# Performance work log

Measured on AMD Instinct MI355X. Metric: run time of the kernel, lower is better.

The kernel has to match this reference:

```python
import jax, jax.numpy as jnp
import numpy as np

# Config derived from layers=[1024,1024,1024,1024,1024]
B = 16384      # batch
H1 = 1024      # layers[1], width of first odd layer (Ux target slice)
SE = 2048      # sum of even-layer dims (0 + 1024 + 1024)
SO = 2048      # sum of odd-layer dims (1024 + 1024)
LAYER = 1024
N_STEPS = 10


def rho(x):
    return jax.nn.sigmoid(4.0 * (x - 0.5))


def rhod(x):
    r = rho(x)
    return 4.0 * r * (1.0 - r)


def _block_mask():
    # Staircase blocks per layer_slices(): (0:1024,0:1024), (0:1024,1024:2048), (1024:2048,1024:2048)
    m = np.zeros((SE, SO), dtype=np.float32)
    m[0:LAYER, 0:LAYER] = 1.0
    m[0:LAYER, LAYER:2 * LAYER] = 1.0
    m[LAYER:2 * LAYER, LAYER:2 * LAYER] = 1.0
    return jnp.asarray(m)


def setup_inputs() -> dict:
    key = jax.random.key(0)
    k1, k2, k3, k4, k5 = jax.random.split(key, 5)
    Ux = jax.random.normal(k1, (B, H1), dtype=jnp.float32)
    s = jax.random.normal(k2, (B, SE + SO), dtype=jnp.float32)
    # Xavier uniform per 1024x1024 block: bound = sqrt(6 / (1024 + 1024))
    bound = (6.0 / (2 * LAYER)) ** 0.5
    W = jax.random.uniform(k3, (SE, SO), minval=-bound, maxval=bound, dtype=jnp.float32) * _block_mask()
    b_even = 0.01 * jax.random.normal(k4, (1, SE), dtype=jnp.float32)
    b_odd = 0.01 * jax.random.normal(k5, (1, SO), dtype=jnp.float32)
    return {"Ux": Ux, "s": s, "W": W, "b_even": b_even, "b_odd": b_odd}


def reference(Ux, s, W, b_even, b_odd):
    s_even, s_odd = s[:, :SE], s[:, SE:]
    # C_odd = rho(s_even) @ W + b_odd ; first odd layer also receives Ux
    C_odd = rho(s_even) @ W + b_odd
    C_odd = C_odd.at[:, :H1].add(Ux)
    for _ in range(N_STEPS):
        s_odd = 0.5 * s_odd + 0.5 * rhod(s_odd) * C_odd
    C_even = rho(s_odd) @ W.T + b_even
    for _ in range(N_STEPS):
        s_even = 0.5 * s_even + 0.5 * rhod(s_even) * C_even
    return jnp.concatenate([s_even, s_odd], axis=-1)
```

## Files before the change

kernel.cpp:

```cpp
#include <hip/hip_runtime.h>
#include <hip/hip_bf16.h>

#define BATCH 16384
#define SEW   2048
#define H1W   1024
#define NSTEP 10

typedef unsigned short u16;
typedef __attribute__((ext_vector_type(8))) __bf16 bf16x8;
typedef __attribute__((ext_vector_type(4))) float   f32x4;

__device__ __forceinline__ void split2(float x, u16& h, u16& l) {
    unsigned u = __float_as_uint(x);
    h = (u16)(u >> 16);
    float hf = __uint_as_float(u & 0xFFFF0000u);
    float r  = x - hf;
    l = (u16)(__float_as_uint(r) >> 16);
}

__device__ __forceinline__ float rho_f(float x) {
    return 1.0f / (1.0f + __expf(2.0f - 4.0f * x));
}

__device__ __forceinline__ void gl2lds16(const u16* g, u16* l) {
    __builtin_amdgcn_global_load_lds(
        (const __attribute__((address_space(1))) void*)g,
        (__attribute__((address_space(3))) void*)l, 16, 0, 0);
}

__global__ void prep_w(const float* __restrict__ W,
                       u16* __restrict__ Whi, u16* __restrict__ Wlo,
                       u16* __restrict__ WThi, u16* __restrict__ WTlo) {
    __shared__ float tile[32][33];
    const int tx = threadIdx.x, ty = threadIdx.y;
    const int x = blockIdx.x * 32 + tx;
#pragma unroll
    for (int k = 0; k < 4; ++k) {
        int y = blockIdx.y * 32 + ty + k * 8;
        float v = W[y * SEW + x];
        tile[ty + k * 8][tx] = v;
        u16 h, l; split2(v, h, l);
        Whi[y * SEW + x] = h; Wlo[y * SEW + x] = l;
    }
    __syncthreads();
#pragma unroll
    for (int k = 0; k < 4; ++k) {
        int r = blockIdx.x * 32 + ty + k * 8;
        int c = blockIdx.y * 32 + tx;
        float v = tile[tx][ty + k * 8];
        u16 h, l; split2(v, h, l);
        WThi[r * SEW + c] = h; WTlo[r * SEW + c] = l;
    }
}

__global__ void prep_rho(const float* __restrict__ s,
                         u16* __restrict__ Rhi, u16* __restrict__ Rlo) {
    int i = blockIdx.x * blockDim.x + threadIdx.x;
    int e = i << 2;
    int row = e >> 11;
    int col = e & 2047;
    const float4 v = *(const float4*)(s + ((size_t)row << 12) + col);
    float xs[4] = {v.x, v.y, v.z, v.w};
    u16 h[4], l[4];
#pragma unroll
    for (int k = 0; k < 4; ++k) {
        float r = rho_f(xs[k]);
        split2(r, h[k], l[k]);
    }
    *(ushort4*)(Rhi + e) = make_ushort4(h[0], h[1], h[2], h[3]);
    *(ushort4*)(Rlo + e) = make_ushort4(l[0], l[1], l[2], l[3]);
}

template <int PHASE>
__global__ __launch_bounds__(256, 2)
void gemm_fused(const u16* __restrict__ Ahi, const u16* __restrict__ Alo,
                const u16* __restrict__ Bhi, const u16* __restrict__ Blo,
                const float* __restrict__ bias,
                const float* __restrict__ Ux,
                const float* __restrict__ s_in,
                float* __restrict__ out,
                u16* __restrict__ R2hi, u16* __restrict__ R2lo) {
    __shared__ u16 lsAh[128 * 32], lsAl[128 * 32], lsBh[128 * 32], lsBl[128 * 32];

    const int tid = threadIdx.x;
    const int m0 = blockIdx.x * 128;
    const int n0 = blockIdx.y * 128;

    int k0, k1;
    if (PHASE == 1) { k0 = 0;                      k1 = (n0 < 1024) ? 1024 : 2048; }
    else            { k0 = (n0 < 1024) ? 0 : 1024; k1 = 2048; }

    const int p0 = tid, p1 = tid + 256;
    const int r0 = p0 >> 2, r1 = p1 >> 2;
    const int g0 = (p0 & 3) ^ ((r0 >> 1) & 3);
    const int g1 = (p1 & 3) ^ ((r1 >> 1) & 3);
    const int aoff0 = (m0 + r0) * SEW + g0 * 8;
    const int aoff1 = (m0 + r1) * SEW + g1 * 8;
    const int boff0 = (n0 + r0) * SEW + g0 * 8;
    const int boff1 = (n0 + r1) * SEW + g1 * 8;

    const int lane = tid & 63;
    const int w = tid >> 6;
    const int wr = w >> 1, wc = w & 1;
    const int q = lane >> 4, lr = lane & 15;
    int offA[4], offB[4];
#pragma unroll
    for (int i = 0; i < 4; ++i) {
        int row = wr * 64 + i * 16 + lr;
        offA[i] = row * 64 + ((q ^ ((row >> 1) & 3)) << 4);
        row = wc * 64 + i * 16 + lr;
        offB[i] = row * 64 + ((q ^ ((row >> 1) & 3)) << 4);
    }

    f32x4 acc[4][4];
    const f32x4 zero = {0.f, 0.f, 0.f, 0.f};
#pragma unroll
    for (int i = 0; i < 4; ++i)
#pragma unroll
        for (int j = 0; j < 4; ++j) acc[i][j] = zero;

    const int nk = (k1 - k0) >> 5;
    for (int kt = 0; kt < nk; ++kt) {
        const int kb = k0 + (kt << 5);
        __syncthreads();
        gl2lds16(Ahi + aoff0 + kb, lsAh + p0 * 8);
        gl2lds16(Ahi + aoff1 + kb, lsAh + p1 * 8);
        gl2lds16(Alo + aoff0 + kb, lsAl + p0 * 8);
        gl2lds16(Alo + aoff1 + kb, lsAl + p1 * 8);
        gl2lds16(Bhi + boff0 + kb, lsBh + p0 * 8);
        gl2lds16(Bhi + boff1 + kb, lsBh + p1 * 8);
        gl2lds16(Blo + boff0 + kb, lsBl + p0 * 8);
        gl2lds16(Blo + boff1 + kb, lsBl + p1 * 8);
        __syncthreads();

        bf16x8 ah[4], al[4], bh[4], bl[4];
#pragma unroll
        for (int i = 0; i < 4; ++i) {
            ah[i] = *(const bf16x8*)((const char*)lsAh + offA[i]);
            al[i] = *(const bf16x8*)((const char*)lsAl + offA[i]);
            bh[i] = *(const bf16x8*)((const char*)lsBh + offB[i]);
            bl[i] = *(const bf16x8*)((const char*)lsBl + offB[i]);
        }
#pragma unroll
        for (int i = 0; i < 4; ++i)
#pragma unroll
            for (int j = 0; j < 4; ++j) {
                acc[i][j] = __builtin_amdgcn_mfma_f32_16x16x32_bf16(ah[i], bh[j], acc[i][j], 0, 0, 0);
                acc[i][j] = __builtin_amdgcn_mfma_f32_16x16x32_bf16(ah[i], bl[j], acc[i][j], 0, 0, 0);
                acc[i][j] = __builtin_amdgcn_mfma_f32_16x16x32_bf16(al[i], bh[j], acc[i][j], 0, 0, 0);
            }
    }

#pragma unroll
    for (int i = 0; i < 4; ++i) {
#pragma unroll
        for (int j = 0; j < 4; ++j) {
            const int col = n0 + wc * 64 + j * 16 + lr;
            const float bv = bias[col];
            float c[4], sv[4];
#pragma unroll
            for (int jj = 0; jj < 4; ++jj) {
                const int row = m0 + wr * 64 + i * 16 + q * 4 + jj;
                c[jj] = acc[i][j][jj] + bv;
                if (PHASE == 1) {
                    if (n0 < 1024) c[jj] += Ux[(size_t)row * H1W + col];
                }
                sv[jj] = s_in[(size_t)row * 4096 + col];
            }
#pragma unroll 1
            for (int t = 0; t < NSTEP; ++t) {
#pragma unroll
                for (int jj = 0; jj < 4; ++jj) {
                    float r  = rho_f(sv[jj]);
                    float rd = 4.0f * r * (1.0f - r);
                    sv[jj] = 0.5f * sv[jj] + 0.5f * rd * c[jj];
                }
            }
#pragma unroll
            for (int jj = 0; jj < 4; ++jj) {
                const int row = m0 + wr * 64 + i * 16 + q * 4 + jj;
                out[(size_t)row * 4096 + col] = sv[jj];
                if (PHASE == 1) {
                    float r = rho_f(sv[jj]);
                    u16 h, l; split2(r, h, l);
                    R2hi[row * SEW + col] = h;
                    R2lo[row * SEW + col] = l;
                }
            }
        }
    }
}

extern "C" void kernel_launch(void* const* d_in, const int* in_sizes, int n_in,
                              void* d_out, int out_size, void* d_ws, size_t ws_size,
                              hipStream_t stream) {
    (void)in_sizes; (void)n_in; (void)out_size; (void)ws_size;
    const float* Ux     = (const float*)d_in[0];
    const float* s      = (const float*)d_in[1];
    const float* W      = (const float*)d_in[2];
    const float* b_even = (const float*)d_in[3];
    const float* b_odd  = (const float*)d_in[4];
    float* out = (float*)d_out;

    char* ws = (char*)d_ws;
    const size_t MB = 1024ull * 1024ull;
    u16* R1hi = (u16*)(ws);
    u16* R1lo = (u16*)(ws + 64 * MB);
    u16* R2hi = (u16*)(ws + 128 * MB);
    u16* R2lo = (u16*)(ws + 192 * MB);
    u16* Whi  = (u16*)(ws + 256 * MB);
    u16* Wlo  = (u16*)(ws + 264 * MB);
    u16* WThi = (u16*)(ws + 272 * MB);
    u16* WTlo = (u16*)(ws + 280 * MB);

    prep_w<<<dim3(64, 64), dim3(32, 8), 0, stream>>>(W, Whi, Wlo, WThi, WTlo);
    prep_rho<<<(BATCH * SEW / 4) / 256, 256, 0, stream>>>(s, R1hi, R1lo);

    gemm_fused<1><<<dim3(128, 16), 256, 0, stream>>>(
        R1hi, R1lo, WThi, WTlo, b_odd, Ux,
        s + SEW, out + SEW, R2hi, R2lo);

    gemm_fused<2><<<dim3(128, 16), 256, 0, stream>>>(
        R2hi, R2lo, Whi, Wlo, b_even, nullptr,
        s, out, nullptr, nullptr);
}
```

Before: 1.378 ms.

## Use 256x256 tiles with double-buffered LDS, K=64 stages and XCD-aware block remap

The fused GEMM moves from 128x128 tiles with 256 threads to 256x256 tiles with 512 threads. Each wave now holds an 8x4 accumulator block, and the K dimension is staged 64 wide through double-buffered LDS. The three hi/lo split products are turned into a stream of virtual K tiles (hi*hi, hi*lo, lo*hi), so each stage loads a single A/B pair and the next stage's loads overlap the current MFMAs via vmcnt waits. A 1D grid is remapped so neighbouring tiles land on the same XCD, and s_setprio is raised around the MFMA bursts. The aim is more data reuse per byte loaded and less barrier stall, at the cost of more registers, 128KB of LDS, fewer blocks and possibly lower occupancy.

Measured after the change: 1.606 ms. 1.17x slower.

```diff
diff --git a/kernel.cpp b/kernel.cpp
--- a/kernel.cpp
+++ b/kernel.cpp
@@ -72,7 +72,7 @@
 }
 
 template <int PHASE>
-__global__ __launch_bounds__(256, 2)
+__global__ __launch_bounds__(512, 2)
 void gemm_fused(const u16* __restrict__ Ahi, const u16* __restrict__ Alo,
                 const u16* __restrict__ Bhi, const u16* __restrict__ Blo,
                 const float* __restrict__ bias,
@@ -80,88 +80,143 @@
                 const float* __restrict__ s_in,
                 float* __restrict__ out,
                 u16* __restrict__ R2hi, u16* __restrict__ R2lo) {
-    __shared__ u16 lsAh[128 * 32], lsAl[128 * 32], lsBh[128 * 32], lsBl[128 * 32];
+    __shared__ u16 ldsA[2][256 * 64];
+    __shared__ u16 ldsB[2][256 * 64];
 
     const int tid = threadIdx.x;
-    const int m0 = blockIdx.x * 128;
-    const int n0 = blockIdx.y * 128;
-
-    int k0, k1;
-    if (PHASE == 1) { k0 = 0;                      k1 = (n0 < 1024) ? 1024 : 2048; }
-    else            { k0 = (n0 < 1024) ? 0 : 1024; k1 = 2048; }
-
-    const int p0 = tid, p1 = tid + 256;
-    const int r0 = p0 >> 2, r1 = p1 >> 2;
-    const int g0 = (p0 & 3) ^ ((r0 >> 1) & 3);
-    const int g1 = (p1 & 3) ^ ((r1 >> 1) & 3);
-    const int aoff0 = (m0 + r0) * SEW + g0 * 8;
-    const int aoff1 = (m0 + r1) * SEW + g1 * 8;
-    const int boff0 = (n0 + r0) * SEW + g0 * 8;
-    const int boff1 = (n0 + r1) * SEW + g1 * 8;
+
+    const int wg = blockIdx.x;
+    const int L  = (wg & 7) * 64 + (wg >> 3);
+    const int m0 = (L >> 3) * 256;
+    const int n0 = (L & 7) * 256;
+
+    int kt0, nkt;
+    if (PHASE == 1) { kt0 = 0;                    nkt = (n0 < 1024) ? 16 : 32; }
+    else            { kt0 = (n0 < 1024) ? 0 : 16; nkt = (n0 < 1024) ? 32 : 16; }
+    const int nvt = 3 * nkt;
+
+    const int srow  = tid >> 3;
+    const int sswz  = (tid >> 4) & 7;
+    const int scol  = ((tid & 7) ^ sswz) * 8;
+    const int aoff0 = (m0 + srow) * SEW + scol;
+    const int boff0 = (n0 + srow) * SEW + scol;
 
     const int lane = tid & 63;
-    const int w = tid >> 6;
-    const int wr = w >> 1, wc = w & 1;
-    const int q = lane >> 4, lr = lane & 15;
-    int offA[4], offB[4];
-#pragma unroll
-    for (int i = 0; i < 4; ++i) {
-        int row = wr * 64 + i * 16 + lr;
-        offA[i] = row * 64 + ((q ^ ((row >> 1) & 3)) << 4);
-        row = wc * 64 + i * 16 + lr;
-        offB[i] = row * 64 + ((q ^ ((row >> 1) & 3)) << 4);
-    }
-
-    f32x4 acc[4][4];
+    const int w  = tid >> 6;
+    const int wr = w >> 2, wc = w & 3;
+    const int lr = lane & 15, q = lane >> 4;
+    const int swz = (lr >> 1) & 7;
+    const int oh0 = ((q)     ^ swz) * 16;
+    const int oh1 = ((4 + q) ^ swz) * 16;
+    const int baseA = (wr * 128 + lr) * 128;
+    const int baseB = (wc * 64  + lr) * 128;
+
+    f32x4 acc[8][4];
     const f32x4 zero = {0.f, 0.f, 0.f, 0.f};
 #pragma unroll
-    for (int i = 0; i < 4; ++i)
+    for (int i = 0; i < 8; ++i)
 #pragma unroll
         for (int j = 0; j < 4; ++j) acc[i][j] = zero;
 
-    const int nk = (k1 - k0) >> 5;
-    for (int kt = 0; kt < nk; ++kt) {
-        const int kb = k0 + (kt << 5);
-        __syncthreads();
-        gl2lds16(Ahi + aoff0 + kb, lsAh + p0 * 8);
-        gl2lds16(Ahi + aoff1 + kb, lsAh + p1 * 8);
-        gl2lds16(Alo + aoff0 + kb, lsAl + p0 * 8);
-        gl2lds16(Alo + aoff1 + kb, lsAl + p1 * 8);
-        gl2lds16(Bhi + boff0 + kb, lsBh + p0 * 8);
-        gl2lds16(Bhi + boff1 + kb, lsBh + p1 * 8);
-        gl2lds16(Blo + boff0 + kb, lsBl + p0 * 8);
-        gl2lds16(Blo + boff1 + kb, lsBl + p1 * 8);
-        __syncthreads();
-
-        bf16x8 ah[4], al[4], bh[4], bl[4];
+#define STAGE(As, Bs, kk, buf) do {                                          \
+        u16* dA_ = &ldsA[buf][tid * 8];                                      \
+        u16* dB_ = &ldsB[buf][tid * 8];                                      \
+        const u16* sa_ = (As) + aoff0 + (kk);                                \
+        const u16* sb_ = (Bs) + boff0 + (kk);                                \
+        _Pragma("unroll")                                                    \
+        for (int i_ = 0; i_ < 4; ++i_) {                                     \
+            gl2lds16(sa_ + i_ * (64 * SEW), dA_ + i_ * 4096);                \
+            gl2lds16(sb_ + i_ * (64 * SEW), dB_ + i_ * 4096);                \
+        }                                                                    \
+    } while (0)
+
+    int skk = kt0 * 64;
+    int st  = 1;
+    STAGE(Ahi, Bhi, skk, 0);
+
+    for (int vt = 0; vt < nvt; ++vt) {
+        const int cur = vt & 1;
+        if (vt + 1 < nvt) {
+            const u16* As = (st < 2)  ? Ahi : Alo;
+            const u16* Bs = (st == 1) ? Blo : Bhi;
+            STAGE(As, Bs, skk, cur ^ 1);
+            if (++st == 3) { st = 0; skk += 64; }
+            asm volatile("s_waitcnt vmcnt(8)" ::: "memory");
+        } else {
+            asm volatile("s_waitcnt vmcnt(0)" ::: "memory");
+        }
+        __builtin_amdgcn_s_barrier();
+
+        const char* la = (const char*)ldsA[cur];
+        const char* lb = (const char*)ldsB[cur];
+        bf16x8 av[4][2], bv[4][2];
 #pragma unroll
         for (int i = 0; i < 4; ++i) {
-            ah[i] = *(const bf16x8*)((const char*)lsAh + offA[i]);
-            al[i] = *(const bf16x8*)((const char*)lsAl + offA[i]);
-            bh[i] = *(const bf16x8*)((const char*)lsBh + offB[i]);
-            bl[i] = *(const bf16x8*)((const char*)lsBl + offB[i]);
-        }
-#pragma unroll
-        for (int i = 0; i < 4; ++i)
-#pragma unroll
-            for (int j = 0; j < 4; ++j) {
-                acc[i][j] = __builtin_amdgcn_mfma_f32_16x16x32_bf16(ah[i], bh[j], acc[i][j], 0, 0, 0);
-                acc[i][j] = __builtin_amdgcn_mfma_f32_16x16x32_bf16(ah[i], bl[j], acc[i][j], 0, 0, 0);
-                acc[i][j] = __builtin_amdgcn_mfma_f32_16x16x32_bf16(al[i], bh[j], acc[i][j], 0, 0, 0);
-            }
-    }
-
-#pragma unroll
-    for (int i = 0; i < 4; ++i) {
+            av[i][0] = *(const bf16x8*)(la + baseA + i * 2048 + oh0);
+            av[i][1] = *(const bf16x8*)(la + baseA + i * 2048 + oh1);
+        }
+#pragma unroll
+        for (int j = 0; j < 4; ++j) {
+            bv[j][0] = *(const bf16x8*)(lb + baseB + j * 2048 + oh0);
+            bv[j][1] = *(const bf16x8*)(lb + baseB + j * 2048 + oh1);
+        }
+        __builtin_amdgcn_s_setprio(1);
+#pragma unroll
+        for (int i = 0; i < 4; ++i)
+#pragma unroll
+            for (int j = 0; j < 2; ++j) {
+                acc[i][j] = __builtin_amdgcn_mfma_f32_16x16x32_bf16(av[i][0], bv[j][0], acc[i][j], 0, 0, 0);
+                acc[i][j] = __builtin_amdgcn_mfma_f32_16x16x32_bf16(av[i][1], bv[j][1], acc[i][j], 0, 0, 0);
+            }
+        __builtin_amdgcn_s_setprio(0);
+        __builtin_amdgcn_s_setprio(1);
+#pragma unroll
+        for (int i = 0; i < 4; ++i)
+#pragma unroll
+            for (int j = 2; j < 4; ++j) {
+                acc[i][j] = __builtin_amdgcn_mfma_f32_16x16x32_bf16(av[i][0], bv[j][0], acc[i][j], 0, 0, 0);
+                acc[i][j] = __builtin_amdgcn_mfma_f32_16x16x32_bf16(av[i][1], bv[j][1], acc[i][j], 0, 0, 0);
+            }
+        __builtin_amdgcn_s_setprio(0);
+#pragma unroll
+        for (int i = 0; i < 4; ++i) {
+            av[i][0] = *(const bf16x8*)(la + baseA + (i + 4) * 2048 + oh0);
+            av[i][1] = *(const bf16x8*)(la + baseA + (i + 4) * 2048 + oh1);
+        }
+        __builtin_amdgcn_s_setprio(1);
+#pragma unroll
+        for (int i = 0; i < 4; ++i)
+#pragma unroll
+            for (int j = 0; j < 2; ++j) {
+                acc[4 + i][j] = __builtin_amdgcn_mfma_f32_16x16x32_bf16(av[i][0], bv[j][0], acc[4 + i][j], 0, 0, 0);
+                acc[4 + i][j] = __builtin_amdgcn_mfma_f32_16x16x32_bf16(av[i][1], bv[j][1], acc[4 + i][j], 0, 0, 0);
+            }
+        __builtin_amdgcn_s_setprio(0);
+        __builtin_amdgcn_s_setprio(1);
+#pragma unroll
+        for (int i = 0; i < 4; ++i)
+#pragma unroll
+            for (int j = 2; j < 4; ++j) {
+                acc[4 + i][j] = __builtin_amdgcn_mfma_f32_16x16x32_bf16(av[i][0], bv[j][0], acc[4 + i][j], 0, 0, 0);
+                acc[4 + i][j] = __builtin_amdgcn_mfma_f32_16x16x32_bf16(av[i][1], bv[j][1], acc[4 + i][j], 0, 0, 0);
+            }
+        __builtin_amdgcn_s_setprio(0);
+
+        __builtin_amdgcn_s_barrier();
+    }
+#undef STAGE
+
+#pragma unroll
+    for (int i = 0; i < 8; ++i) {
 #pragma unroll
         for (int j = 0; j < 4; ++j) {
             const int col = n0 + wc * 64 + j * 16 + lr;
-            const float bv = bias[col];
+            const float bvv = bias[col];
             float c[4], sv[4];
 #pragma unroll
             for (int jj = 0; jj < 4; ++jj) {
-                const int row = m0 + wr * 64 + i * 16 + q * 4 + jj;
-                c[jj] = acc[i][j][jj] + bv;
+                const int row = m0 + wr * 128 + i * 16 + q * 4 + jj;
+                c[jj] = acc[i][j][jj] + bvv;
                 if (PHASE == 1) {
                     if (n0 < 1024) c[jj] += Ux[(size_t)row * H1W + col];
                 }
@@ -178,13 +233,13 @@
             }
 #pragma unroll
             for (int jj = 0; jj < 4; ++jj) {
-                const int row = m0 + wr * 64 + i * 16 + q * 4 + jj;
+                const int row = m0 + wr * 128 + i * 16 + q * 4 + jj;
                 out[(size_t)row * 4096 + col] = sv[jj];
                 if (PHASE == 1) {
                     float r = rho_f(sv[jj]);
                     u16 h, l; split2(r, h, l);
-                    R2hi[row * SEW + col] = h;
-                    R2lo[row * SEW + col] = l;
+                    R2hi[(size_t)row * SEW + col] = h;
+                    R2lo[(size_t)row * SEW + col] = l;
                 }
             }
         }
@@ -216,11 +271,11 @@
     prep_w<<<dim3(64, 64), dim3(32, 8), 0, stream>>>(W, Whi, Wlo, WThi, WTlo);
     prep_rho<<<(BATCH * SEW / 4) / 256, 256, 0, stream>>>(s, R1hi, R1lo);
 
-    gemm_fused<1><<<dim3(128, 16), 256, 0, stream>>>(
+    gemm_fused<1><<<dim3(512), 512, 0, stream>>>(
         R1hi, R1lo, WThi, WTlo, b_odd, Ux,
         s + SEW, out + SEW, R2hi, R2lo);
 
-    gemm_fused<2><<<dim3(128, 16), 256, 0, stream>>>(
+    gemm_fused<2><<<dim3(512), 512, 0, stream>>>(
         R2hi, R2lo, Whi, Wlo, b_even, nullptr,
         s, out, nullptr, nullptr);
 }
```
